# Kernel optimization log

Measured on AMD Instinct MI355X. Metric: run time of the kernel, lower is better.

## Reference

```python
import jax, jax.numpy as jnp
import numpy as np

B, M, N_CTR, K = 16, 2048, 512, 32
DIM, DEPTH, HEADS = 384, 6, 6
EMB = 48  # fourier embedding dim (48//6 = 8 freqs per axis, basis [3,24])


def make_basis():
    e = (2.0 ** np.arange(EMB // 6)).astype(np.float32) * np.pi  # [8]
    z = np.zeros(EMB // 6, np.float32)
    basis = np.stack([np.concatenate([e, z, z]),
                      np.concatenate([z, e, z]),
                      np.concatenate([z, z, e])])  # [3, 24]
    return jnp.asarray(basis)


def fourier_embed(x, basis):
    # x [..., 3] -> [..., 48]  (sin/cos of 24 frequency projections)
    p = jnp.einsum('...d,de->...e', x, basis)
    return jnp.concatenate([jnp.sin(p), jnp.cos(p)], axis=-1)


def fps_idx(pos, n):
    # farthest point sampling, deterministic start at index 0. pos [M,3] -> [n]
    d0 = jnp.sum((pos - pos[0]) ** 2, -1)
    def step(d, _):
        i = jnp.argmax(d)
        d = jnp.minimum(d, jnp.sum((pos - pos[i]) ** 2, -1))
        return d, i
    _, idxs = jax.lax.scan(step, d0, None, length=n - 1)
    return jnp.concatenate([jnp.zeros(1, jnp.int32), idxs.astype(jnp.int32)])


def layernorm(x, g, b, eps=1e-6):
    m = jnp.mean(x, -1, keepdims=True)
    v = jnp.var(x, -1, keepdims=True)
    return (x - m) * jax.lax.rsqrt(v + eps) * g + b


def _lin(key, fi, fo):
    kw, kb = jax.random.split(key)
    w = jax.random.normal(kw, (fi, fo), jnp.float32) / np.sqrt(fi)
    b = jax.random.normal(kb, (fo,), jnp.float32) * 0.01
    return w, b


def setup_inputs() -> dict:
    key = jax.random.key(0)
    ks = jax.random.split(key, 16)
    pc = jax.random.uniform(ks[0], (B, M, 3), jnp.float32)
    embed_w, embed_b = _lin(ks[1], 3 + EMB, DIM)
    lw1, lb1 = _lin(ks[2], 3 + EMB, 256)
    lw2, lb2 = _lin(ks[3], 256, 256)
    gw1, gb1 = _lin(ks[4], 256, 256)
    gw2, gb2 = _lin(ks[5], 256, DIM)
    def stack_lin(k, fi, fo):
        kk = jax.random.split(k, DEPTH)
        ws, bs = zip(*[_lin(kk[i], fi, fo) for i in range(DEPTH)])
        return jnp.stack(ws), jnp.stack(bs)
    qkv_w, qkv_b = stack_lin(ks[6], DIM, 3 * DIM)
    proj_w, proj_b = stack_lin(ks[7], DIM, DIM)
    fc1_w, fc1_b = stack_lin(ks[8], DIM, 4 * DIM)
    fc2_w, fc2_b = stack_lin(ks[9], 4 * DIM, DIM)
    return dict(
        pc=pc, embed_w=embed_w, embed_b=embed_b,
        lw1=lw1, lb1=lb1, lw2=lw2, lb2=lb2,
        gw1=gw1, gb1=gb1, gw2=gw2, gb2=gb2,
        ln1_g=jnp.ones((DEPTH, DIM)), ln1_b=jnp.zeros((DEPTH, DIM)),
        qkv_w=qkv_w, qkv_b=qkv_b, proj_w=proj_w, proj_b=proj_b,
        gamma1=jax.random.normal(ks[10], (DEPTH, DIM)) * 0.1,
        ln2_g=jnp.ones((DEPTH, DIM)), ln2_b=jnp.zeros((DEPTH, DIM)),
        fc1_w=fc1_w, fc1_b=fc1_b, fc2_w=fc2_w, fc2_b=fc2_b,
        gamma2=jax.random.normal(ks[11], (DEPTH, DIM)) * 0.1,
        lnf_g=jnp.ones((DIM,)), lnf_b=jnp.zeros((DIM,)),
    )


def reference(pc, embed_w, embed_b, lw1, lb1, lw2, lb2, gw1, gb1, gw2, gb2,
              ln1_g, ln1_b, qkv_w, qkv_b, proj_w, proj_b, gamma1,
              ln2_g, ln2_b, fc1_w, fc1_b, fc2_w, fc2_b, gamma2, lnf_g, lnf_b):
    basis = make_basis()
    # --- FPS centers (per batch) ---
    idx = jax.vmap(lambda p: fps_idx(p, N_CTR))(pc)                 # [B,N]
    centers = jnp.take_along_axis(pc, idx[:, :, None], axis=1)      # [B,N,3]
    # --- KNN graph: for each center, K nearest of the M points ---
    d2 = jnp.sum((centers[:, :, None, :] - pc[:, None, :, :]) ** 2, -1)  # [B,N,M]
    _, nn_idx = jax.lax.top_k(-d2, K)                               # [B,N,K]
    # --- PointConv: gather -> local MLP -> max-scatter -> global MLP ---
    src = jax.vmap(lambda p, i: p[i])(pc, nn_idx)                   # [B,N,K,3]
    rel = src - centers[:, :, None, :]
    feat = jnp.concatenate([rel, fourier_embed(rel, basis)], -1)    # [B,N,K,51]
    h = jax.nn.relu(feat @ lw1 + lb1) @ lw2 + lb2                   # [B,N,K,256]
    h = jnp.max(h, axis=2)  # scatter_max over edges == max over K neighbors
    x = jax.nn.relu(h @ gw1 + gb1) @ gw2 + gb2                      # [B,N,DIM]
    # --- positional embedding tokens ---
    pe = jnp.concatenate([centers, fourier_embed(centers, basis)], -1) @ embed_w + embed_b
    x = x + pe
    # --- ViT blocks (pre-LN, LayerScale, eval mode: no dropout/droppath) ---
    hd = DIM // HEADS
    scale = hd ** -0.5
    for l in range(DEPTH):
        xn = layernorm(x, ln1_g[l], ln1_b[l])
        qkv = (xn @ qkv_w[l] + qkv_b[l]).reshape(B, N_CTR, 3, HEADS, hd)
        q, k, v = jnp.moveaxis(qkv, 2, 0)                           # [B,N,H,hd]
        att = jax.nn.softmax(jnp.einsum('bqhd,bkhd->bhqk', q, k) * scale, axis=-1)
        o = jnp.einsum('bhqk,bkhd->bqhd', att, v).reshape(B, N_CTR, DIM)
        x = x + gamma1[l] * (o @ proj_w[l] + proj_b[l])
        xn = layernorm(x, ln2_g[l], ln2_b[l])
        mlp = jax.nn.gelu(xn @ fc1_w[l] + fc1_b[l], approximate=False) @ fc2_w[l] + fc2_b[l]
        x = x + gamma2[l] * mlp
    out = layernorm(x, lnf_g, lnf_b)
    return out, centers
```

## Files before the change

### kernel.cpp

```cpp
#include <hip/hip_runtime.h>
#include <math.h>

#define NB 16
#define NM 2048
#define NCTR 512
#define NK 32
#define NDIM 384

typedef unsigned long long ull;
typedef unsigned int uint;
typedef unsigned short ushort;
typedef __attribute__((ext_vector_type(8))) short bf16x8;
typedef __attribute__((ext_vector_type(4))) float f32x4;

__device__ __forceinline__ float dist2_exact(float ax, float ay, float az,
                                             float bx, float by, float bz) {
  float dx = __fsub_rn(ax, bx);
  float dy = __fsub_rn(ay, by);
  float dz = __fsub_rn(az, bz);
  return __fadd_rn(__fadd_rn(__fmul_rn(dx, dx), __fmul_rn(dy, dy)),
                   __fmul_rn(dz, dz));
}

__device__ __forceinline__ float gelu_f(float x) {
  return 0.5f * x * (1.0f + erff(x * 0.70710678118654752f));
}

__device__ __forceinline__ ushort f2bf(float f) {
  uint u = __float_as_uint(f);
  return (ushort)((u + 0x7FFFu + ((u >> 16) & 1u)) >> 16);
}
__device__ __forceinline__ float bf2f(ushort h) {
  return __uint_as_float(((uint)h) << 16);
}

__device__ __forceinline__ void cvt8(float4 p, float4 q, uint4& hi, uint4& lo) {
  float v0 = p.x, v1 = p.y, v2 = p.z, v3 = p.w;
  float v4 = q.x, v5 = q.y, v6 = q.z, v7 = q.w;
  ushort h0 = f2bf(v0), h1 = f2bf(v1), h2 = f2bf(v2), h3 = f2bf(v3);
  ushort h4 = f2bf(v4), h5 = f2bf(v5), h6 = f2bf(v6), h7 = f2bf(v7);
  ushort l0 = f2bf(v0 - bf2f(h0)), l1 = f2bf(v1 - bf2f(h1));
  ushort l2 = f2bf(v2 - bf2f(h2)), l3 = f2bf(v3 - bf2f(h3));
  ushort l4 = f2bf(v4 - bf2f(h4)), l5 = f2bf(v5 - bf2f(h5));
  ushort l6 = f2bf(v6 - bf2f(h6)), l7 = f2bf(v7 - bf2f(h7));
  hi.x = (uint)h0 | ((uint)h1 << 16); hi.y = (uint)h2 | ((uint)h3 << 16);
  hi.z = (uint)h4 | ((uint)h5 << 16); hi.w = (uint)h6 | ((uint)h7 << 16);
  lo.x = (uint)l0 | ((uint)l1 << 16); lo.y = (uint)l2 | ((uint)l3 << 16);
  lo.z = (uint)l4 | ((uint)l5 << 16); lo.w = (uint)l6 | ((uint)l7 << 16);
}

__device__ __forceinline__ void split_store(float v, ushort* H, ushort* L,
                                            size_t off) {
  ushort hi = f2bf(v);
  H[off] = hi;
  L[off] = f2bf(v - bf2f(hi));
}

struct WAll {
  const float* src[8];
  ushort* dst[8];
  int K8[8];
  int N[8];
  int Ksrc[8];
  int blk0[9];
};

__global__ __launch_bounds__(256)
void fps_wconv(const float* __restrict__ pc, float* __restrict__ centers,
               WAll a) {
  __shared__ float4 pos4[NM];
  __shared__ ull red[2][4];
  if (blockIdx.x >= 16) {
    int bid = blockIdx.x - 16;
    int f = 0;
#pragma unroll
    for (int i = 1; i < 8; ++i) f += (bid >= a.blk0[i]);
    int K8 = a.K8[f], N = a.N[f], Ksrc = a.Ksrc[f];
    int c = (bid - a.blk0[f]) * 256 + threadIdx.x;
    if (c >= K8 * N) return;
    const float* W = a.src[f];
    ushort* out = a.dst[f];
    int kb = c / N, n = c - kb * N;
    float v[8];
#pragma unroll
    for (int i = 0; i < 8; ++i) {
      int row = kb * 8 + i;
      v[i] = (row < Ksrc) ? W[(size_t)row * N + n] : 0.f;
    }
    float4 p, q;
    p.x = v[0]; p.y = v[1]; p.z = v[2]; p.w = v[3];
    q.x = v[4]; q.y = v[5]; q.z = v[6]; q.w = v[7];
    uint4 hi, lo;
    cvt8(p, q, hi, lo);
    *(uint4*)(out + (size_t)c * 8) = hi;
    *(uint4*)(out + (size_t)(K8 * N + c) * 8) = lo;
    return;
  }
  int b = blockIdx.x;
  const float* pb = pc + (size_t)b * (NM * 3);
  int tid = threadIdx.x, lane = tid & 63, wv = tid >> 6;
  float px[8], py[8], pz[8];
#pragma unroll
  for (int i = 0; i < 8; ++i) {
    int p = tid + 256 * i;
    float x = pb[3 * p], y = pb[3 * p + 1], z = pb[3 * p + 2];
    px[i] = x; py[i] = y; pz[i] = z;
    pos4[p] = make_float4(x, y, z, 0.f);
  }
  __syncthreads();
  float* cb = centers + (size_t)b * (NCTR * 3);
  float4 s0 = pos4[0];
  float sx = s0.x, sy = s0.y, sz = s0.z;
  if (tid == 0) { cb[0] = sx; cb[1] = sy; cb[2] = sz; }
  float d[8];
  for (int n = 1; n < NCTR; ++n) {
    ull best = 0;
#pragma unroll
    for (int i = 0; i < 8; ++i) {
      int p = tid + 256 * i;
      float nd = dist2_exact(px[i], py[i], pz[i], sx, sy, sz);
      d[i] = (n == 1) ? nd : fminf(d[i], nd);
      ull key = ((ull)__float_as_uint(d[i]) << 32) | (unsigned)(0x7FFFFFFF - p);
      best = best > key ? best : key;
    }
    float dl = __uint_as_float((uint)(best >> 32));
    float wm = dl;
#pragma unroll
    for (int off = 32; off; off >>= 1) wm = fmaxf(wm, __shfl_xor(wm, off));
    ull mask = __ballot(dl == wm);
    ull wkey;
    if (mask & (mask - 1)) {
      wkey = best;
#pragma unroll
      for (int off = 32; off; off >>= 1) {
        ull o = __shfl_xor(wkey, off);
        wkey = wkey > o ? wkey : o;
      }
    } else {
      int src = __ffsll((long long)mask) - 1;
      wkey = __shfl(best, src);
    }
    if (lane == 0) red[n & 1][wv] = wkey;
    __syncthreads();
    ull g0 = red[n & 1][0], g1 = red[n & 1][1];
    ull g2 = red[n & 1][2], g3 = red[n & 1][3];
    ull ga = g0 > g1 ? g0 : g1;
    ull gc2 = g2 > g3 ? g2 : g3;
    ull gb = ga > gc2 ? ga : gc2;
    int j = 0x7FFFFFFF - (int)(unsigned)(gb & 0xFFFFFFFFull);
    float4 np = pos4[j];
    sx = np.x; sy = np.y; sz = np.z;
    if (tid == 0) { cb[n * 3] = sx; cb[n * 3 + 1] = sy; cb[n * 3 + 2] = sz; }
  }
}

__global__ __launch_bounds__(256, 2)
void knn_kernel(const float* __restrict__ pc, const float* __restrict__ centers,
                int* __restrict__ nn) {
  __shared__ float pos[NM * 3];
  int b = blockIdx.x >> 7;
  int n0 = (blockIdx.x & 127) << 2;
  const float* pb = pc + (size_t)b * (NM * 3);
  for (int i = threadIdx.x; i < NM * 3; i += 256) pos[i] = pb[i];
  __syncthreads();
  int wv = threadIdx.x >> 6, lane = threadIdx.x & 63;
  int gc = b * NCTR + n0 + wv;
  float cx = centers[gc * 3], cy = centers[gc * 3 + 1], cz = centers[gc * 3 + 2];
  ull key[32];
  ull gmin[4];
#pragma unroll
  for (int g = 0; g < 4; ++g) {
    gmin[g] = ~0ull;
#pragma unroll
    for (int i = 0; i < 8; ++i) {
      int r = g * 8 + i;
      int p = lane + (r << 6);
      float nd = dist2_exact(pos[3 * p], pos[3 * p + 1], pos[3 * p + 2], cx, cy, cz);
      key[r] = ((ull)__float_as_uint(nd) << 11) | (unsigned)p;
      gmin[g] = gmin[g] < key[r] ? gmin[g] : key[r];
    }
  }
  ull a01 = gmin[0] < gmin[1] ? gmin[0] : gmin[1];
  ull a23 = gmin[2] < gmin[3] ? gmin[2] : gmin[3];
  ull lmin = a01 < a23 ? a01 : a23;
  int* nnc = nn + (size_t)gc * NK;
  for (int round = 0; round < NK; ++round) {
    ull w = lmin;
#pragma unroll
    for (int off = 32; off; off >>= 1) {
      ull o = __shfl_xor(w, off);
      w = w < o ? w : o;
    }
    if (lmin == w) {
      nnc[round] = (int)(w & 2047ull);
#pragma unroll
      for (int g = 0; g < 4; ++g) {
        if (gmin[g] == w) {
          gmin[g] = ~0ull;
#pragma unroll
          for (int i = 0; i < 8; ++i) {
            int r = g * 8 + i;
            key[r] = (key[r] == w) ? ~0ull : key[r];
            gmin[g] = gmin[g] < key[r] ? gmin[g] : key[r];
          }
        }
      }
      ull b01 = gmin[0] < gmin[1] ? gmin[0] : gmin[1];
      ull b23 = gmin[2] < gmin[3] ? gmin[2] : gmin[3];
      lmin = b01 < b23 ? b01 : b23;
    }
  }
}

__global__ __launch_bounds__(256, 2)
void edge_mfma(const float* __restrict__ pc, const float* __restrict__ centers,
               const int* __restrict__ nn, const ushort* __restrict__ lw1s,
               const float* __restrict__ lb1, const ushort* __restrict__ lw2s,
               const float* __restrict__ lb2, ushort* __restrict__ hH,
               ushort* __restrict__ hL) {
  __shared__ __align__(16) ushort featH[4096], featL[4096];
  __shared__ __align__(16) ushort t1H[16384], t1L[16384];
  int tid = threadIdx.x;
  int w = tid >> 6, lane = tid & 63;
  int l15 = lane & 15, l4 = lane >> 4;
  int wbase = w << 6;
  {
    int e = tid >> 2, s = tid & 3;
    int ge = blockIdx.x * 64 + e;
    int c = ge >> 5;
    int b = c >> 9;
    int j = nn[ge];
    const float* sp = pc + ((size_t)b * NM + j) * 3;
    float rx = sp[0] - centers[c * 3];
    float ry = sp[1] - centers[c * 3 + 1];
    float rz = sp[2] - centers[c * 3 + 2];
    auto putk = [&](int k, float v) {
      ushort hi = f2bf(v);
      ushort lo = f2bf(v - bf2f(hi));
      int idx = ((k >> 3) * 64 + e) * 8 + (k & 7);
      featH[idx] = hi;
      featL[idx] = lo;
    };
    if (s < 3) {
      float r = (s == 0) ? rx : (s == 1) ? ry : rz;
#pragma unroll
      for (int f = 0; f < 8; ++f) {
        float ef = (float)(M_PI * (double)(1 << f));
        float p = r * ef;
        putk(3 + 8 * s + f, sinf(p));
        putk(27 + 8 * s + f, cosf(p));
      }
    } else {
      putk(0, rx);
      putk(1, ry);
      putk(2, rz);
#pragma unroll
      for (int k = 51; k < 64; ++k) putk(k, 0.f);
    }
  }
  __syncthreads();
  const ushort* lw1H = lw1s;
  const ushort* lw1L = lw1s + 8 * 256 * 8;
  f32x4 acc1[4][4];
#pragma unroll
  for (int i = 0; i < 4; ++i)
#pragma unroll
    for (int j = 0; j < 4; ++j) acc1[i][j] = (f32x4){0.f, 0.f, 0.f, 0.f};
#pragma unroll
  for (int ks = 0; ks < 2; ++ks) {
    bf16x8 ah[4], al[4];
#pragma unroll
    for (int fm = 0; fm < 4; ++fm) {
      int idx = ((ks * 4 + l4) * 64 + fm * 16 + l15) * 8;
      ah[fm] = *(const bf16x8*)&featH[idx];
      al[fm] = *(const bf16x8*)&featL[idx];
    }
#pragma unroll
    for (int fn = 0; fn < 4; ++fn) {
      int col = wbase + fn * 16 + l15;
      size_t boff = ((size_t)(ks * 4 + l4) * 256 + col) * 8;
      bf16x8 bh = *(const bf16x8*)(lw1H + boff);
      bf16x8 bl = *(const bf16x8*)(lw1L + boff);
#pragma unroll
      for (int fm = 0; fm < 4; ++fm) {
        acc1[fm][fn] = __builtin_amdgcn_mfma_f32_16x16x32_bf16(al[fm], bh, acc1[fm][fn], 0, 0, 0);
        acc1[fm][fn] = __builtin_amdgcn_mfma_f32_16x16x32_bf16(ah[fm], bl, acc1[fm][fn], 0, 0, 0);
        acc1[fm][fn] = __builtin_amdgcn_mfma_f32_16x16x32_bf16(ah[fm], bh, acc1[fm][fn], 0, 0, 0);
      }
    }
  }
#pragma unroll
  for (int fn = 0; fn < 4; ++fn) {
    int chan = wbase + fn * 16 + l15;
    float bias = lb1[chan];
    int kb = chan >> 3, k7 = chan & 7;
#pragma unroll
    for (int fm = 0; fm < 4; ++fm) {
#pragma unroll
      for (int r = 0; r < 4; ++r) {
        int edge = fm * 16 + l4 * 4 + r;
        float v = fmaxf(acc1[fm][fn][r] + bias, 0.f);
        ushort hi = f2bf(v);
        ushort lo = f2bf(v - bf2f(hi));
        int idx = (kb * 64 + edge) * 8 + k7;
        t1H[idx] = hi;
        t1L[idx] = lo;
      }
    }
  }
  __syncthreads();
  const ushort* lw2H = lw2s;
  const ushort* lw2L = lw2s + 32 * 256 * 8;
  f32x4 acc2[4][4];
#pragma unroll
  for (int i = 0; i < 4; ++i)
#pragma unroll
    for (int j = 0; j < 4; ++j) acc2[i][j] = (f32x4){0.f, 0.f, 0.f, 0.f};
#pragma unroll
  for (int ks = 0; ks < 8; ++ks) {
    bf16x8 ah[4], al[4];
#pragma unroll
    for (int fm = 0; fm < 4; ++fm) {
      int idx = ((ks * 4 + l4) * 64 + fm * 16 + l15) * 8;
      ah[fm] = *(const bf16x8*)&t1H[idx];
      al[fm] = *(const bf16x8*)&t1L[idx];
    }
#pragma unroll
    for (int fn = 0; fn < 4; ++fn) {
      int col = wbase + fn * 16 + l15;
      size_t boff = ((size_t)(ks * 4 + l4) * 256 + col) * 8;
      bf16x8 bh = *(const bf16x8*)(lw2H + boff);
      bf16x8 bl = *(const bf16x8*)(lw2L + boff);
#pragma unroll
      for (int fm = 0; fm < 4; ++fm) {
        acc2[fm][fn] = __builtin_amdgcn_mfma_f32_16x16x32_bf16(al[fm], bh, acc2[fm][fn], 0, 0, 0);
        acc2[fm][fn] = __builtin_amdgcn_mfma_f32_16x16x32_bf16(ah[fm], bl, acc2[fm][fn], 0, 0, 0);
        acc2[fm][fn] = __builtin_amdgcn_mfma_f32_16x16x32_bf16(ah[fm], bh, acc2[fm][fn], 0, 0, 0);
      }
    }
  }
#pragma unroll
  for (int fn = 0; fn < 4; ++fn) {
    int col = wbase + fn * 16 + l15;
    float m0 = -INFINITY, m1 = -INFINITY;
#pragma unroll
    for (int r = 0; r < 4; ++r) {
      m0 = fmaxf(m0, fmaxf(acc2[0][fn][r], acc2[1][fn][r]));
      m1 = fmaxf(m1, fmaxf(acc2[2][fn][r], acc2[3][fn][r]));
    }
    m0 = fmaxf(m0, __shfl_xor(m0, 16));
    m0 = fmaxf(m0, __shfl_xor(m0, 32));
    m1 = fmaxf(m1, __shfl_xor(m1, 16));
    m1 = fmaxf(m1, __shfl_xor(m1, 32));
    if (l4 == 0) {
      float bias = lb2[col];
      int c0 = blockIdx.x * 2;
      split_store(m0 + bias, hH, hL, (size_t)c0 * 256 + col);
      split_store(m1 + bias, hH, hL, (size_t)(c0 + 1) * 256 + col);
    }
  }
}

template <int EPI, int OUTS, int BM>
__global__ __launch_bounds__(256, 2)
void gemm_s(const ushort* __restrict__ AH, const ushort* __restrict__ AL,
            const ushort* __restrict__ Wh, const ushort* __restrict__ Wl,
            const float* __restrict__ bias, const float* __restrict__ gamma,
            const float* __restrict__ resid, float* __restrict__ C,
            ushort* __restrict__ CH, ushort* __restrict__ CL,
            int M, int N, int K) {
  constexpr int FN = (BM == 128) ? 4 : 2;
  __shared__ __align__(16) ushort Ah[BM * 32], Al[BM * 32];
  __shared__ __align__(16) ushort Bh[4096], Bl[4096];
  int tid = threadIdx.x;
  int bn = blockIdx.x << 7, bm = blockIdx.y * BM;
  int wid = tid >> 6, lane = tid & 63;
  int wr = (BM == 128) ? (wid >> 1) : 0;
  int wc = (BM == 128) ? (wid & 1) : wid;
  int l15 = lane & 15, l4 = lane >> 4;

  int arow = (BM == 128) ? (tid >> 1) : (tid & 63);
  int akb0 = (BM == 128) ? ((tid & 1) << 1) : (tid >> 6);
  const ushort* ApH = AH + (size_t)(bm + arow) * K + akb0 * 8;
  const ushort* ApL = AL + (size_t)(bm + arow) * K + akb0 * 8;
  int wkb = tid >> 7, wn = tid & 127;

  f32x4 acc[4][FN];
#pragma unroll
  for (int i = 0; i < 4; ++i)
#pragma unroll
    for (int j = 0; j < FN; ++j) acc[i][j] = (f32x4){0.f, 0.f, 0.f, 0.f};

  uint4 aH0 = *(const uint4*)(ApH);
  uint4 aL0 = *(const uint4*)(ApL);
  uint4 aH1, aL1;
  if (BM == 128) {
    aH1 = *(const uint4*)(ApH + 8);
    aL1 = *(const uint4*)(ApL + 8);
  }
  size_t wo1 = ((size_t)wkb * N + bn + wn) * 8;
  size_t wo2 = ((size_t)(wkb + 2) * N + bn + wn) * 8;
  uint4 w0 = *(const uint4*)(Wh + wo1);
  uint4 w1 = *(const uint4*)(Wh + wo2);
  uint4 w2 = *(const uint4*)(Wl + wo1);
  uint4 w3 = *(const uint4*)(Wl + wo2);

  int nkt = K >> 5;
  for (int kt = 0; kt < nkt; ++kt) {
    if (BM == 128) {
      *(uint4*)&Ah[(akb0 * 128 + arow) * 8] = aH0;
      *(uint4*)&Ah[((akb0 + 1) * 128 + arow) * 8] = aH1;
      *(uint4*)&Al[(akb0 * 128 + arow) * 8] = aL0;
      *(uint4*)&Al[((akb0 + 1) * 128 + arow) * 8] = aL1;
    } else {
      *(uint4*)&Ah[(akb0 * 64 + arow) * 8] = aH0;
      *(uint4*)&Al[(akb0 * 64 + arow) * 8] = aL0;
    }
    *(uint4*)&Bh[tid * 8] = w0;
    *(uint4*)&Bh[(tid + 256) * 8] = w1;
    *(uint4*)&Bl[tid * 8] = w2;
    *(uint4*)&Bl[(tid + 256) * 8] = w3;
    __syncthreads();
    if (kt + 1 < nkt) {
      aH0 = *(const uint4*)(ApH + (kt + 1) * 32);
      aL0 = *(const uint4*)(ApL + (kt + 1) * 32);
      if (BM == 128) {
        aH1 = *(const uint4*)(ApH + (kt + 1) * 32 + 8);
        aL1 = *(const uint4*)(ApL + (kt + 1) * 32 + 8);
      }
      size_t b1 = ((size_t)((kt + 1) * 4 + wkb) * N + bn + wn) * 8;
      size_t b2 = ((size_t)((kt + 1) * 4 + wkb + 2) * N + bn + wn) * 8;
      w0 = *(const uint4*)(Wh + b1);
      w1 = *(const uint4*)(Wh + b2);
      w2 = *(const uint4*)(Wl + b1);
      w3 = *(const uint4*)(Wl + b2);
    }
    bf16x8 ahf[4], alf[4];
#pragma unroll
    for (int fm = 0; fm < 4; ++fm) {
      int ci = l4 * BM + wr * 64 + fm * 16 + l15;
      ahf[fm] = *(bf16x8*)&Ah[ci * 8];
      alf[fm] = *(bf16x8*)&Al[ci * 8];
    }
#pragma unroll
    for (int fn = 0; fn < FN; ++fn) {
      int ci = l4 * 128 + wc * (FN * 16) + fn * 16 + l15;
      bf16x8 bh = *(bf16x8*)&Bh[ci * 8];
      bf16x8 bl = *(bf16x8*)&Bl[ci * 8];
#pragma unroll
      for (int fm = 0; fm < 4; ++fm) {
        acc[fm][fn] = __builtin_amdgcn_mfma_f32_16x16x32_bf16(alf[fm], bh, acc[fm][fn], 0, 0, 0);
        acc[fm][fn] = __builtin_amdgcn_mfma_f32_16x16x32_bf16(ahf[fm], bl, acc[fm][fn], 0, 0, 0);
        acc[fm][fn] = __builtin_amdgcn_mfma_f32_16x16x32_bf16(ahf[fm], bh, acc[fm][fn], 0, 0, 0);
      }
    }
    __syncthreads();
  }

#pragma unroll
  for (int fn = 0; fn < FN; ++fn) {
    int col = bn + wc * (FN * 16) + fn * 16 + l15;
    float bv = bias[col];
    float gv = (EPI == 3) ? gamma[col] : 0.f;
#pragma unroll
    for (int fm = 0; fm < 4; ++fm) {
      int row0 = bm + wr * 64 + fm * 16 + l4 * 4;
#pragma unroll
      for (int r = 0; r < 4; ++r) {
        float v = acc[fm][fn][r] + bv;
        if (EPI == 1) v = fmaxf(v, 0.f);
        else if (EPI == 2) v = gelu_f(v);
        else if (EPI == 3) v = resid[(size_t)(row0 + r) * N + col] + gv * v;
        size_t off = (size_t)(row0 + r) * N + col;
        if (OUTS == 0) C[off] = v;
        else split_store(v, CH, CL, off);
      }
    }
  }
}

__global__ __launch_bounds__(256)
void pe_add(const float* __restrict__ centers, const float* __restrict__ ew,
            const float* __restrict__ eb, float* x) {
  __shared__ float fc[51];
  int c = blockIdx.x, tid = threadIdx.x;
  if (tid < 24) {
    int a = tid >> 3, f = tid & 7;
    float coord = centers[c * 3 + a];
    float p = coord * (float)(M_PI * (double)(1 << f));
    fc[3 + tid] = sinf(p);
    fc[27 + tid] = cosf(p);
  } else if (tid < 27) {
    fc[tid - 24] = centers[c * 3 + (tid - 24)];
  }
  __syncthreads();
  for (int j = tid; j < NDIM; j += 256) {
    float acc = eb[j];
#pragma unroll
    for (int d = 0; d < 51; ++d) acc = fmaf(fc[d], ew[d * NDIM + j], acc);
    x[(size_t)c * NDIM + j] += acc;
  }
}

__global__ __launch_bounds__(256)
void ln_f32(const float* __restrict__ x, const float* __restrict__ g,
            const float* __restrict__ b, float* __restrict__ y) {
  int row = (blockIdx.x << 2) + (threadIdx.x >> 6);
  int lane = threadIdx.x & 63;
  const float* xr = x + (size_t)row * NDIM;
  float v[6];
#pragma unroll
  for (int i = 0; i < 6; ++i) v[i] = xr[lane + (i << 6)];
  float s = 0.f;
#pragma unroll
  for (int i = 0; i < 6; ++i) s += v[i];
#pragma unroll
  for (int off = 32; off; off >>= 1) s += __shfl_xor(s, off);
  float m = s / 384.f;
  float var = 0.f;
#pragma unroll
  for (int i = 0; i < 6; ++i) { float dd = v[i] - m; var += dd * dd; }
#pragma unroll
  for (int off = 32; off; off >>= 1) var += __shfl_xor(var, off);
  var = var / 384.f;
  float rs = 1.f / sqrtf(var + 1e-6f);
#pragma unroll
  for (int i = 0; i < 6; ++i) {
    int cc = lane + (i << 6);
    y[(size_t)row * NDIM + cc] = (v[i] - m) * rs * g[cc] + b[cc];
  }
}

__global__ __launch_bounds__(256)
void ln_split(const float* __restrict__ x, const float* __restrict__ g,
              const float* __restrict__ b, ushort* __restrict__ yH,
              ushort* __restrict__ yL) {
  int row = (blockIdx.x << 2) + (threadIdx.x >> 6);
  int lane = threadIdx.x & 63;
  const float* xr = x + (size_t)row * NDIM;
  float v[6];
#pragma unroll
  for (int i = 0; i < 6; ++i) v[i] = xr[lane + (i << 6)];
  float s = 0.f;
#pragma unroll
  for (int i = 0; i < 6; ++i) s += v[i];
#pragma unroll
  for (int off = 32; off; off >>= 1) s += __shfl_xor(s, off);
  float m = s / 384.f;
  float var = 0.f;
#pragma unroll
  for (int i = 0; i < 6; ++i) { float dd = v[i] - m; var += dd * dd; }
#pragma unroll
  for (int off = 32; off; off >>= 1) var += __shfl_xor(var, off);
  var = var / 384.f;
  float rs = 1.f / sqrtf(var + 1e-6f);
#pragma unroll
  for (int i = 0; i < 6; ++i) {
    int cc = lane + (i << 6);
    float yv = (v[i] - m) * rs * g[cc] + b[cc];
    split_store(yv, yH, yL, (size_t)row * NDIM + cc);
  }
}

__global__ __launch_bounds__(256, 2)
void attn_mfma(const ushort* __restrict__ FH, const ushort* __restrict__ FL,
               ushort* __restrict__ oH, ushort* __restrict__ oL) {
  __shared__ __align__(16) ushort kTH[4096], kTL[4096];
  __shared__ __align__(16) ushort vSH[4096], vSL[4096];
  __shared__ __align__(16) ushort pSH[8192], pSL[8192];
  int bi = blockIdx.x;
  int qt = bi & 3;
  int hh = (bi >> 2) % 6;
  int b = bi / 24;
  int tid = threadIdx.x;
  int w = tid >> 6, lane = tid & 63;
  int l15 = lane & 15, l4 = lane >> 4;
  const ushort* baseH = FH + (size_t)(b * NCTR) * 1152;
  const ushort* baseL = FL + (size_t)(b * NCTR) * 1152;
  int qbase = qt * 128 + w * 32;

  bf16x8 qh[2][2], ql[2][2];
#pragma unroll
  for (int qr = 0; qr < 2; ++qr) {
#pragma unroll
    for (int ds = 0; ds < 2; ++ds) {
      size_t off = (size_t)(qbase + qr * 16 + l15) * 1152 + hh * 64 + ds * 32 + l4 * 8;
      qh[qr][ds] = *(const bf16x8*)(baseH + off);
      ql[qr][ds] = *(const bf16x8*)(baseL + off);
    }
  }

  f32x4 oacc[2][4];
#pragma unroll
  for (int i = 0; i < 2; ++i)
#pragma unroll
    for (int j = 0; j < 4; ++j) oacc[i][j] = (f32x4){0.f, 0.f, 0.f, 0.f};
  float m_[2][4], l_[2][4];
#pragma unroll
  for (int i = 0; i < 2; ++i)
#pragma unroll
    for (int r = 0; r < 4; ++r) { m_[i][r] = -INFINITY; l_[i][r] = 0.f; }

  ushort* pHw = pSH + w * 2048;
  ushort* pLw = pSL + w * 2048;

  for (int ch = 0; ch < 8; ++ch) {
    {
      int key = tid & 63, dgh = tid >> 6;
      size_t krow = (size_t)(ch * 64 + key) * 1152 + 384 + hh * 64;
#pragma unroll
      for (int i = 0; i < 2; ++i) {
        int dg = dgh * 2 + i;
        *(uint4*)&kTH[(dg * 64 + key) * 8] = *(const uint4*)(baseH + krow + dg * 8);
        *(uint4*)&kTL[(dg * 64 + key) * 8] = *(const uint4*)(baseL + krow + dg * 8);
      }
      int d = tid & 63, kb2 = tid >> 6;
#pragma unroll
      for (int i = 0; i < 2; ++i) {
        int kb = kb2 + i * 4;
        ushort hv[8], lv[8];
#pragma unroll
        for (int j = 0; j < 8; ++j) {
          size_t off = (size_t)(ch * 64 + kb * 8 + j) * 1152 + 768 + hh * 64 + d;
          hv[j] = baseH[off];
          lv[j] = baseL[off];
        }
        uint4 H, L;
        H.x = (uint)hv[0] | ((uint)hv[1] << 16); H.y = (uint)hv[2] | ((uint)hv[3] << 16);
        H.z = (uint)hv[4] | ((uint)hv[5] << 16); H.w = (uint)hv[6] | ((uint)hv[7] << 16);
        L.x = (uint)lv[0] | ((uint)lv[1] << 16); L.y = (uint)lv[2] | ((uint)lv[3] << 16);
        L.z = (uint)lv[4] | ((uint)lv[5] << 16); L.w = (uint)lv[6] | ((uint)lv[7] << 16);
        *(uint4*)&vSH[(kb * 64 + d) * 8] = H;
        *(uint4*)&vSL[(kb * 64 + d) * 8] = L;
      }
    }
    __syncthreads();

    f32x4 sacc[2][4];
#pragma unroll
    for (int i = 0; i < 2; ++i)
#pragma unroll
      for (int j = 0; j < 4; ++j) sacc[i][j] = (f32x4){0.f, 0.f, 0.f, 0.f};
#pragma unroll
    for (int ds = 0; ds < 2; ++ds) {
#pragma unroll
      for (int kc = 0; kc < 4; ++kc) {
        int idx = ((ds * 4 + l4) * 64 + kc * 16 + l15) * 8;
        bf16x8 bh = *(const bf16x8*)&kTH[idx];
        bf16x8 bl = *(const bf16x8*)&kTL[idx];
#pragma unroll
        for (int qr = 0; qr < 2; ++qr) {
          sacc[qr][kc] = __builtin_amdgcn_mfma_f32_16x16x32_bf16(ql[qr][ds], bh, sacc[qr][kc], 0, 0, 0);
          sacc[qr][kc] = __builtin_amdgcn_mfma_f32_16x16x32_bf16(qh[qr][ds], bl, sacc[qr][kc], 0, 0, 0);
          sacc[qr][kc] = __builtin_amdgcn_mfma_f32_16x16x32_bf16(qh[qr][ds], bh, sacc[qr][kc], 0, 0, 0);
        }
      }
    }

    float t[2][4];
#pragma unroll
    for (int qr = 0; qr < 2; ++qr)
#pragma unroll
      for (int r = 0; r < 4; ++r) {
        float a0 = sacc[qr][0][r] * 0.125f; sacc[qr][0][r] = a0;
        float a1 = sacc[qr][1][r] * 0.125f; sacc[qr][1][r] = a1;
        float a2 = sacc[qr][2][r] * 0.125f; sacc[qr][2][r] = a2;
        float a3 = sacc[qr][3][r] * 0.125f; sacc[qr][3][r] = a3;
        t[qr][r] = fmaxf(fmaxf(a0, a1), fmaxf(a2, a3));
      }
#pragma unroll
    for (int off = 1; off < 16; off <<= 1)
#pragma unroll
      for (int qr = 0; qr < 2; ++qr)
#pragma unroll
        for (int r = 0; r < 4; ++r)
          t[qr][r] = fmaxf(t[qr][r], __shfl_xor(t[qr][r], off));
    float f_[2][4];
#pragma unroll
    for (int qr = 0; qr < 2; ++qr)
#pragma unroll
      for (int r = 0; r < 4; ++r) {
        float mn = fmaxf(m_[qr][r], t[qr][r]);
        f_[qr][r] = expf(m_[qr][r] - mn);
        m_[qr][r] = mn;
      }
#pragma unroll
    for (int qr = 0; qr < 2; ++qr)
#pragma unroll
      for (int dc = 0; dc < 4; ++dc)
#pragma unroll
        for (int r = 0; r < 4; ++r) oacc[qr][dc][r] *= f_[qr][r];
    float sm[2][4];
#pragma unroll
    for (int qr = 0; qr < 2; ++qr)
#pragma unroll
      for (int r = 0; r < 4; ++r) {
        float p0 = expf(sacc[qr][0][r] - m_[qr][r]); sacc[qr][0][r] = p0;
        float p1 = expf(sacc[qr][1][r] - m_[qr][r]); sacc[qr][1][r] = p1;
        float p2 = expf(sacc[qr][2][r] - m_[qr][r]); sacc[qr][2][r] = p2;
        float p3 = expf(sacc[qr][3][r] - m_[qr][r]); sacc[qr][3][r] = p3;
        sm[qr][r] = ((p0 + p1) + (p2 + p3));
      }
#pragma unroll
    for (int off = 1; off < 16; off <<= 1)
#pragma unroll
      for (int qr = 0; qr < 2; ++qr)
#pragma unroll
        for (int r = 0; r < 4; ++r)
          sm[qr][r] += __shfl_xor(sm[qr][r], off);
#pragma unroll
    for (int qr = 0; qr < 2; ++qr)
#pragma unroll
      for (int r = 0; r < 4; ++r) l_[qr][r] = l_[qr][r] * f_[qr][r] + sm[qr][r];

#pragma unroll
    for (int qr = 0; qr < 2; ++qr)
#pragma unroll
      for (int kc = 0; kc < 4; ++kc)
#pragma unroll
        for (int r = 0; r < 4; ++r) {
          float pv = sacc[qr][kc][r];
          ushort hi = f2bf(pv);
          ushort lo = f2bf(pv - bf2f(hi));
          int k = kc * 16 + l15;
          int qrow = qr * 16 + l4 * 4 + r;
          int idx = ((k >> 3) * 32 + qrow) * 8 + (k & 7);
          pHw[idx] = hi;
          pLw[idx] = lo;
        }

#pragma unroll
    for (int ks = 0; ks < 2; ++ks) {
      bf16x8 pah[2], pal[2];
#pragma unroll
      for (int qr = 0; qr < 2; ++qr) {
        int idx = ((ks * 4 + l4) * 32 + qr * 16 + l15) * 8;
        pah[qr] = *(const bf16x8*)&pHw[idx];
        pal[qr] = *(const bf16x8*)&pLw[idx];
      }
#pragma unroll
      for (int dc = 0; dc < 4; ++dc) {
        int idx = ((ks * 4 + l4) * 64 + dc * 16 + l15) * 8;
        bf16x8 vh = *(const bf16x8*)&vSH[idx];
        bf16x8 vl = *(const bf16x8*)&vSL[idx];
#pragma unroll
        for (int qr = 0; qr < 2; ++qr) {
          oacc[qr][dc] = __builtin_amdgcn_mfma_f32_16x16x32_bf16(pal[qr], vh, oacc[qr][dc], 0, 0, 0);
          oacc[qr][dc] = __builtin_amdgcn_mfma_f32_16x16x32_bf16(pah[qr], vl, oacc[qr][dc], 0, 0, 0);
          oacc[qr][dc] = __builtin_amdgcn_mfma_f32_16x16x32_bf16(pah[qr], vh, oacc[qr][dc], 0, 0, 0);
        }
      }
    }
    __syncthreads();
  }

  float il[2][4];
#pragma unroll
  for (int qr = 0; qr < 2; ++qr)
#pragma unroll
    for (int r = 0; r < 4; ++r) il[qr][r] = 1.f / l_[qr][r];
#pragma unroll
  for (int qr = 0; qr < 2; ++qr)
#pragma unroll
    for (int dc = 0; dc < 4; ++dc)
#pragma unroll
      for (int r = 0; r < 4; ++r) {
        int row = b * NCTR + qbase + qr * 16 + l4 * 4 + r;
        int col = hh * 64 + dc * 16 + l15;
        split_store(oacc[qr][dc][r] * il[qr][r], oH, oL, (size_t)row * NDIM + col);
      }
}

extern "C" void kernel_launch(void* const* d_in, const int* in_sizes, int n_in,
                              void* d_out, int out_size, void* d_ws, size_t ws_size,
                              hipStream_t stream) {
  const float* pc      = (const float*)d_in[0];
  const float* embed_w = (const float*)d_in[1];
  const float* embed_b = (const float*)d_in[2];
  const float* lw1     = (const float*)d_in[3];
  const float* lb1     = (const float*)d_in[4];
  const float* lw2     = (const float*)d_in[5];
  const float* lb2     = (const float*)d_in[6];
  const float* gw1     = (const float*)d_in[7];
  const float* gb1     = (const float*)d_in[8];
  const float* gw2     = (const float*)d_in[9];
  const float* gb2     = (const float*)d_in[10];
  const float* ln1_g   = (const float*)d_in[11];
  const float* ln1_b   = (const float*)d_in[12];
  const float* qkv_w   = (const float*)d_in[13];
  const float* qkv_b   = (const float*)d_in[14];
  const float* proj_w  = (const float*)d_in[15];
  const float* proj_b  = (const float*)d_in[16];
  const float* gamma1  = (const float*)d_in[17];
  const float* ln2_g   = (const float*)d_in[18];
  const float* ln2_b   = (const float*)d_in[19];
  const float* fc1_w   = (const float*)d_in[20];
  const float* fc1_b   = (const float*)d_in[21];
  const float* fc2_w   = (const float*)d_in[22];
  const float* fc2_b   = (const float*)d_in[23];
  const float* gamma2  = (const float*)d_in[24];
  const float* lnf_g   = (const float*)d_in[25];
  const float* lnf_b   = (const float*)d_in[26];

  float* out = (float*)d_out;
  float* centers = out + (size_t)NB * NCTR * NDIM;

  char* ws = (char*)d_ws;
  int*    nn  = (int*)(ws + 0);
  float*  x   = (float*)(ws + 1048576);
  ushort* xnH = (ushort*)(ws + 13631488);
  ushort* xnL = (ushort*)(ws + 19922944);
  ushort* FH  = (ushort*)(ws + 26214400);
  ushort* FL  = (ushort*)(ws + 51380224);
  ushort* hH  = (ushort*)(ws + 76546048);
  ushort* hL  = (ushort*)(ws + 80740352);
  ushort* wsplit = (ushort*)(ws + 84934656);

  WAll wa;
  const float* srcs[8] = {qkv_w, proj_w, fc1_w, fc2_w, gw1, gw2, lw1, lw2};
  int kpads[8] = {2304, 2304, 2304, 9216, 256, 256, 64, 256};
  int ns[8]    = {1152, 384, 1536, 384, 256, 384, 256, 256};
  int ksrcs[8] = {2304, 2304, 2304, 9216, 256, 256, 51, 256};
  ushort* dsts[8];
  size_t wofs = 0;
  int cum = 0;
  for (int f = 0; f < 8; ++f) {
    dsts[f] = wsplit + wofs;
    wofs += (size_t)2 * kpads[f] * ns[f];
    wa.src[f] = srcs[f];
    wa.dst[f] = dsts[f];
    wa.K8[f] = kpads[f] >> 3;
    wa.N[f] = ns[f];
    wa.Ksrc[f] = ksrcs[f];
    wa.blk0[f] = cum;
    cum += ((kpads[f] >> 3) * ns[f] + 255) / 256;
  }
  wa.blk0[8] = cum;
  ushort* qkvS = dsts[0];
  ushort* projS = dsts[1];
  ushort* fc1S = dsts[2];
  ushort* fc2S = dsts[3];
  ushort* g1S = dsts[4];
  ushort* g2S = dsts[5];
  ushort* lw1s = dsts[6];
  ushort* lw2s = dsts[7];

  fps_wconv<<<16 + cum, 256, 0, stream>>>(pc, centers, wa);
  knn_kernel<<<2048, 256, 0, stream>>>(pc, centers, nn);
  edge_mfma<<<4096, 256, 0, stream>>>(pc, centers, nn, lw1s, lb1, lw2s, lb2, hH, hL);

  gemm_s<1, 1, 64><<<dim3(2, 128), 256, 0, stream>>>(
      hH, hL, g1S, g1S + 65536, gb1, nullptr, nullptr, nullptr, xnH, xnL,
      8192, 256, 256);
  gemm_s<0, 0, 64><<<dim3(3, 128), 256, 0, stream>>>(
      xnH, xnL, g2S, g2S + 98304, gb2, nullptr, nullptr, x, nullptr, nullptr,
      8192, 384, 256);
  pe_add<<<8192, 256, 0, stream>>>(centers, embed_w, embed_b, x);

  for (int l = 0; l < 6; ++l) {
    ln_split<<<2048, 256, 0, stream>>>(x, ln1_g + l * 384, ln1_b + l * 384, xnH, xnL);
    gemm_s<0, 1, 128><<<dim3(9, 64), 256, 0, stream>>>(
        xnH, xnL, qkvS + (size_t)l * 442368, qkvS + 2654208 + (size_t)l * 442368,
        qkv_b + l * 1152, nullptr, nullptr, nullptr, FH, FL, 8192, 1152, 384);
    attn_mfma<<<384, 256, 0, stream>>>(FH, FL, xnH, xnL);
    gemm_s<3, 0, 64><<<dim3(3, 128), 256, 0, stream>>>(
        xnH, xnL, projS + (size_t)l * 147456, projS + 884736 + (size_t)l * 147456,
        proj_b + l * 384, gamma1 + l * 384, x, x, nullptr, nullptr, 8192, 384, 384);
    ln_split<<<2048, 256, 0, stream>>>(x, ln2_g + l * 384, ln2_b + l * 384, xnH, xnL);
    gemm_s<2, 1, 128><<<dim3(12, 64), 256, 0, stream>>>(
        xnH, xnL, fc1S + (size_t)l * 589824, fc1S + 3538944 + (size_t)l * 589824,
        fc1_b + l * 1536, nullptr, nullptr, nullptr, FH, FL, 8192, 1536, 384);
    gemm_s<3, 0, 64><<<dim3(3, 128), 256, 0, stream>>>(
        FH, FL, fc2S + (size_t)l * 589824, fc2S + 3538944 + (size_t)l * 589824,
        fc2_b + l * 384, gamma2 + l * 384, x, x, nullptr, nullptr, 8192, 384, 1536);
  }
  ln_f32<<<2048, 256, 0, stream>>>(x, lnf_g, lnf_b, out);
}
```

Before: 1.985 ms.

## Fuse LayerNorm into QKV and FC1 GEMMs, reading fp32 activations directly

Removes the separate ln_split kernels and adds a gemm_ln kernel. Each block computes per-row mean and variance for its 128 rows, then normalizes and splits the fp32 input into hi/lo bf16 while staging the A tile in shared memory. This saves a kernel launch and the write and read of the bf16 normalized buffers twice per layer. In exchange every column block re-reads the fp32 rows and recomputes the statistics (9 or 12 times per row), variance now uses E[x^2]-m^2 which is less numerically robust, and the A load is fp32, so twice the bytes of bf16.

```diff
diff --git a/kernel.cpp b/kernel.cpp
--- a/kernel.cpp
+++ b/kernel.cpp
@@ -479,6 +479,157 @@
   }
 }
 
+template <int EPI>
+__global__ __launch_bounds__(256, 2)
+void gemm_ln(const float* __restrict__ X, const float* __restrict__ lng,
+             const float* __restrict__ lnb,
+             const ushort* __restrict__ Wh, const ushort* __restrict__ Wl,
+             const float* __restrict__ bias,
+             ushort* __restrict__ CH, ushort* __restrict__ CL, int N) {
+  constexpr int K = 384;
+  __shared__ __align__(16) ushort Ah[4096], Al[4096], Bh[4096], Bl[4096];
+  __shared__ __align__(16) float gS[384], bS[384];
+  __shared__ float mS[128], rS[128], redS[512];
+  int tid = threadIdx.x;
+  int bn = blockIdx.x << 7, bm = blockIdx.y << 7;
+  int wid = tid >> 6, lane = tid & 63;
+  int wr = wid >> 1, wc = wid & 1;
+  int l15 = lane & 15, l4 = lane >> 4;
+
+  {
+    const float* xr = X + (size_t)(bm + (tid >> 1)) * K + (tid & 1) * 192;
+    float s = 0.f, s2 = 0.f;
+#pragma unroll
+    for (int i = 0; i < 48; ++i) {
+      float4 v = *(const float4*)(xr + i * 4);
+      s += ((v.x + v.y) + (v.z + v.w));
+      s2 += ((v.x * v.x + v.y * v.y) + (v.z * v.z + v.w * v.w));
+    }
+    redS[tid] = s;
+    redS[256 + tid] = s2;
+    for (int i = tid; i < 384; i += 256) { gS[i] = lng[i]; bS[i] = lnb[i]; }
+    __syncthreads();
+    if (tid < 128) {
+      float st = redS[2 * tid] + redS[2 * tid + 1];
+      float q = redS[256 + 2 * tid] + redS[256 + 2 * tid + 1];
+      float m = st / 384.f;
+      float var = q / 384.f - m * m;
+      mS[tid] = m;
+      rS[tid] = 1.f / sqrtf(var + 1e-6f);
+    }
+    __syncthreads();
+  }
+
+  int arow = tid >> 1, akb0 = (tid & 1) << 1;
+  const float* Ap = X + (size_t)(bm + arow) * K + (akb0 << 3);
+  float rowm = mS[arow], rowr = rS[arow];
+  int wkb = tid >> 7, wn = tid & 127;
+
+  f32x4 acc[4][4];
+#pragma unroll
+  for (int i = 0; i < 4; ++i)
+#pragma unroll
+    for (int j = 0; j < 4; ++j) acc[i][j] = (f32x4){0.f, 0.f, 0.f, 0.f};
+
+  float4 a0 = *(const float4*)(Ap + 0);
+  float4 a1 = *(const float4*)(Ap + 4);
+  float4 a2 = *(const float4*)(Ap + 8);
+  float4 a3 = *(const float4*)(Ap + 12);
+  size_t wo1 = ((size_t)wkb * N + bn + wn) * 8;
+  size_t wo2 = ((size_t)(wkb + 2) * N + bn + wn) * 8;
+  uint4 w0 = *(const uint4*)(Wh + wo1);
+  uint4 w1 = *(const uint4*)(Wh + wo2);
+  uint4 w2 = *(const uint4*)(Wl + wo1);
+  uint4 w3 = *(const uint4*)(Wl + wo2);
+
+  constexpr int nkt = K >> 5;
+  for (int kt = 0; kt < nkt; ++kt) {
+    int kb = kt * 32 + (akb0 << 3);
+    float4 g0 = *(const float4*)&gS[kb],     g1v = *(const float4*)&gS[kb + 4];
+    float4 g2v = *(const float4*)&gS[kb + 8], g3v = *(const float4*)&gS[kb + 12];
+    float4 b0 = *(const float4*)&bS[kb],     b1v = *(const float4*)&bS[kb + 4];
+    float4 b2v = *(const float4*)&bS[kb + 8], b3v = *(const float4*)&bS[kb + 12];
+    float4 n0, n1, n2, n3;
+    n0.x = (a0.x - rowm) * rowr * g0.x + b0.x;
+    n0.y = (a0.y - rowm) * rowr * g0.y + b0.y;
+    n0.z = (a0.z - rowm) * rowr * g0.z + b0.z;
+    n0.w = (a0.w - rowm) * rowr * g0.w + b0.w;
+    n1.x = (a1.x - rowm) * rowr * g1v.x + b1v.x;
+    n1.y = (a1.y - rowm) * rowr * g1v.y + b1v.y;
+    n1.z = (a1.z - rowm) * rowr * g1v.z + b1v.z;
+    n1.w = (a1.w - rowm) * rowr * g1v.w + b1v.w;
+    n2.x = (a2.x - rowm) * rowr * g2v.x + b2v.x;
+    n2.y = (a2.y - rowm) * rowr * g2v.y + b2v.y;
+    n2.z = (a2.z - rowm) * rowr * g2v.z + b2v.z;
+    n2.w = (a2.w - rowm) * rowr * g2v.w + b2v.w;
+    n3.x = (a3.x - rowm) * rowr * g3v.x + b3v.x;
+    n3.y = (a3.y - rowm) * rowr * g3v.y + b3v.y;
+    n3.z = (a3.z - rowm) * rowr * g3v.z + b3v.z;
+    n3.w = (a3.w - rowm) * rowr * g3v.w + b3v.w;
+    uint4 h0, l0, h1, l1;
+    cvt8(n0, n1, h0, l0);
+    cvt8(n2, n3, h1, l1);
+    *(uint4*)&Ah[(akb0 * 128 + arow) * 8] = h0;
+    *(uint4*)&Ah[((akb0 + 1) * 128 + arow) * 8] = h1;
+    *(uint4*)&Al[(akb0 * 128 + arow) * 8] = l0;
+    *(uint4*)&Al[((akb0 + 1) * 128 + arow) * 8] = l1;
+    *(uint4*)&Bh[tid * 8] = w0;
+    *(uint4*)&Bh[(tid + 256) * 8] = w1;
+    *(uint4*)&Bl[tid * 8] = w2;
+    *(uint4*)&Bl[(tid + 256) * 8] = w3;
+    __syncthreads();
+    if (kt + 1 < nkt) {
+      const float* Apn = Ap + (kt + 1) * 32;
+      a0 = *(const float4*)(Apn + 0);
+      a1 = *(const float4*)(Apn + 4);
+      a2 = *(const float4*)(Apn + 8);
+      a3 = *(const float4*)(Apn + 12);
+      size_t c1 = ((size_t)((kt + 1) * 4 + wkb) * N + bn + wn) * 8;
+      size_t c2 = ((size_t)((kt + 1) * 4 + wkb + 2) * N + bn + wn) * 8;
+      w0 = *(const uint4*)(Wh + c1);
+      w1 = *(const uint4*)(Wh + c2);
+      w2 = *(const uint4*)(Wl + c1);
+      w3 = *(const uint4*)(Wl + c2);
+    }
+    bf16x8 ahf[4], alf[4];
+#pragma unroll
+    for (int fm = 0; fm < 4; ++fm) {
+      int ci = l4 * 128 + wr * 64 + fm * 16 + l15;
+      ahf[fm] = *(bf16x8*)&Ah[ci * 8];
+      alf[fm] = *(bf16x8*)&Al[ci * 8];
+    }
+#pragma unroll
+    for (int fn = 0; fn < 4; ++fn) {
+      int ci = l4 * 128 + wc * 64 + fn * 16 + l15;
+      bf16x8 bh = *(bf16x8*)&Bh[ci * 8];
+      bf16x8 bl = *(bf16x8*)&Bl[ci * 8];
+#pragma unroll
+      for (int fm = 0; fm < 4; ++fm) {
+        acc[fm][fn] = __builtin_amdgcn_mfma_f32_16x16x32_bf16(alf[fm], bh, acc[fm][fn], 0, 0, 0);
+        acc[fm][fn] = __builtin_amdgcn_mfma_f32_16x16x32_bf16(ahf[fm], bl, acc[fm][fn], 0, 0, 0);
+        acc[fm][fn] = __builtin_amdgcn_mfma_f32_16x16x32_bf16(ahf[fm], bh, acc[fm][fn], 0, 0, 0);
+      }
+    }
+    __syncthreads();
+  }
+
+#pragma unroll
+  for (int fn = 0; fn < 4; ++fn) {
+    int col = bn + wc * 64 + fn * 16 + l15;
+    float bv = bias[col];
+#pragma unroll
+    for (int fm = 0; fm < 4; ++fm) {
+      int row0 = bm + wr * 64 + fm * 16 + l4 * 4;
+#pragma unroll
+      for (int r = 0; r < 4; ++r) {
+        float v = acc[fm][fn][r] + bv;
+        if (EPI == 2) v = gelu_f(v);
+        split_store(v, CH, CL, (size_t)(row0 + r) * N + col);
+      }
+    }
+  }
+}
+
 __global__ __launch_bounds__(256)
 void pe_add(const float* __restrict__ centers, const float* __restrict__ ew,
             const float* __restrict__ eb, float* x) {
@@ -528,37 +679,6 @@
   for (int i = 0; i < 6; ++i) {
     int cc = lane + (i << 6);
     y[(size_t)row * NDIM + cc] = (v[i] - m) * rs * g[cc] + b[cc];
-  }
-}
-
-__global__ __launch_bounds__(256)
-void ln_split(const float* __restrict__ x, const float* __restrict__ g,
-              const float* __restrict__ b, ushort* __restrict__ yH,
-              ushort* __restrict__ yL) {
-  int row = (blockIdx.x << 2) + (threadIdx.x >> 6);
-  int lane = threadIdx.x & 63;
-  const float* xr = x + (size_t)row * NDIM;
-  float v[6];
-#pragma unroll
-  for (int i = 0; i < 6; ++i) v[i] = xr[lane + (i << 6)];
-  float s = 0.f;
-#pragma unroll
-  for (int i = 0; i < 6; ++i) s += v[i];
-#pragma unroll
-  for (int off = 32; off; off >>= 1) s += __shfl_xor(s, off);
-  float m = s / 384.f;
-  float var = 0.f;
-#pragma unroll
-  for (int i = 0; i < 6; ++i) { float dd = v[i] - m; var += dd * dd; }
-#pragma unroll
-  for (int off = 32; off; off >>= 1) var += __shfl_xor(var, off);
-  var = var / 384.f;
-  float rs = 1.f / sqrtf(var + 1e-6f);
-#pragma unroll
-  for (int i = 0; i < 6; ++i) {
-    int cc = lane + (i << 6);
-    float yv = (v[i] - m) * rs * g[cc] + b[cc];
-    split_store(yv, yH, yL, (size_t)row * NDIM + cc);
   }
 }
 
@@ -858,18 +978,18 @@
   pe_add<<<8192, 256, 0, stream>>>(centers, embed_w, embed_b, x);
 
   for (int l = 0; l < 6; ++l) {
-    ln_split<<<2048, 256, 0, stream>>>(x, ln1_g + l * 384, ln1_b + l * 384, xnH, xnL);
-    gemm_s<0, 1, 128><<<dim3(9, 64), 256, 0, stream>>>(
-        xnH, xnL, qkvS + (size_t)l * 442368, qkvS + 2654208 + (size_t)l * 442368,
-        qkv_b + l * 1152, nullptr, nullptr, nullptr, FH, FL, 8192, 1152, 384);
+    gemm_ln<0><<<dim3(9, 64), 256, 0, stream>>>(
+        x, ln1_g + l * 384, ln1_b + l * 384,
+        qkvS + (size_t)l * 442368, qkvS + 2654208 + (size_t)l * 442368,
+        qkv_b + l * 1152, FH, FL, 1152);
     attn_mfma<<<384, 256, 0, stream>>>(FH, FL, xnH, xnL);
     gemm_s<3, 0, 64><<<dim3(3, 128), 256, 0, stream>>>(
         xnH, xnL, projS + (size_t)l * 147456, projS + 884736 + (size_t)l * 147456,
         proj_b + l * 384, gamma1 + l * 384, x, x, nullptr, nullptr, 8192, 384, 384);
-    ln_split<<<2048, 256, 0, stream>>>(x, ln2_g + l * 384, ln2_b + l * 384, xnH, xnL);
-    gemm_s<2, 1, 128><<<dim3(12, 64), 256, 0, stream>>>(
-        xnH, xnL, fc1S + (size_t)l * 589824, fc1S + 3538944 + (size_t)l * 589824,
-        fc1_b + l * 1536, nullptr, nullptr, nullptr, FH, FL, 8192, 1536, 384);
+    gemm_ln<2><<<dim3(12, 64), 256, 0, stream>>>(
+        x, ln2_g + l * 384, ln2_b + l * 384,
+        fc1S + (size_t)l * 589824, fc1S + 3538944 + (size_t)l * 589824,
+        fc1_b + l * 1536, FH, FL, 1536);
     gemm_s<3, 0, 64><<<dim3(3, 128), 256, 0, stream>>>(
         FH, FL, fc2S + (size_t)l * 589824, fc2S + 3538944 + (size_t)l * 589824,
         fc2_b + l * 384, gamma2 + l * 384, x, x, nullptr, nullptr, 8192, 384, 1536);
```

New measurement: 2.206 ms. +11.1%, slower.

## Run farthest point sampling in a single wavefront per batch to drop block barriers

Applied to the files above, without the earlier changes.

Farthest point sampling now uses one 64-lane wavefront per batch, each lane holding 32 points in registers, so the per-iteration cross-wave shared-memory reduction and __syncthreads disappear. The argmax is tracked as a float plus index with lowest-index tie-breaking instead of packed 64-bit keys. The weight-conversion blocks sharing the launch are resized to 64 threads. The cost is four times more serial distance work per lane on the critical path and higher register pressure, with launch_bounds set to one block.

```diff
diff --git a/kernel.cpp b/kernel.cpp
--- a/kernel.cpp
+++ b/kernel.cpp
@@ -65,18 +65,17 @@
   int blk0[9];
 };
 
-__global__ __launch_bounds__(256)
+__global__ __launch_bounds__(64, 1)
 void fps_wconv(const float* __restrict__ pc, float* __restrict__ centers,
                WAll a) {
   __shared__ float4 pos4[NM];
-  __shared__ ull red[2][4];
   if (blockIdx.x >= 16) {
     int bid = blockIdx.x - 16;
     int f = 0;
 #pragma unroll
     for (int i = 1; i < 8; ++i) f += (bid >= a.blk0[i]);
     int K8 = a.K8[f], N = a.N[f], Ksrc = a.Ksrc[f];
-    int c = (bid - a.blk0[f]) * 256 + threadIdx.x;
+    int c = (bid - a.blk0[f]) * 64 + threadIdx.x;
     if (c >= K8 * N) return;
     const float* W = a.src[f];
     ushort* out = a.dst[f];
@@ -97,60 +96,51 @@
     return;
   }
   int b = blockIdx.x;
+  int lane = threadIdx.x;
   const float* pb = pc + (size_t)b * (NM * 3);
-  int tid = threadIdx.x, lane = tid & 63, wv = tid >> 6;
-  float px[8], py[8], pz[8];
-#pragma unroll
-  for (int i = 0; i < 8; ++i) {
-    int p = tid + 256 * i;
+  float px[32], py[32], pz[32], d[32];
+#pragma unroll
+  for (int i = 0; i < 32; ++i) {
+    int p = lane + (i << 6);
     float x = pb[3 * p], y = pb[3 * p + 1], z = pb[3 * p + 2];
     px[i] = x; py[i] = y; pz[i] = z;
     pos4[p] = make_float4(x, y, z, 0.f);
   }
-  __syncthreads();
   float* cb = centers + (size_t)b * (NCTR * 3);
   float4 s0 = pos4[0];
   float sx = s0.x, sy = s0.y, sz = s0.z;
-  if (tid == 0) { cb[0] = sx; cb[1] = sy; cb[2] = sz; }
-  float d[8];
+  if (lane == 0) { cb[0] = sx; cb[1] = sy; cb[2] = sz; }
   for (int n = 1; n < NCTR; ++n) {
-    ull best = 0;
-#pragma unroll
-    for (int i = 0; i < 8; ++i) {
-      int p = tid + 256 * i;
+    float dmax = -INFINITY;
+    int idx = 0;
+#pragma unroll
+    for (int i = 0; i < 32; ++i) {
+      int p = lane + (i << 6);
       float nd = dist2_exact(px[i], py[i], pz[i], sx, sy, sz);
       d[i] = (n == 1) ? nd : fminf(d[i], nd);
-      ull key = ((ull)__float_as_uint(d[i]) << 32) | (unsigned)(0x7FFFFFFF - p);
-      best = best > key ? best : key;
-    }
-    float dl = __uint_as_float((uint)(best >> 32));
-    float wm = dl;
+      bool gt = d[i] > dmax;
+      dmax = gt ? d[i] : dmax;
+      idx = gt ? p : idx;
+    }
+    float wm = dmax;
 #pragma unroll
     for (int off = 32; off; off >>= 1) wm = fmaxf(wm, __shfl_xor(wm, off));
-    ull mask = __ballot(dl == wm);
-    ull wkey;
+    ull mask = __ballot(dmax == wm);
+    int widx;
     if (mask & (mask - 1)) {
-      wkey = best;
+      int cand = (dmax == wm) ? idx : 0x7FFFFFFF;
 #pragma unroll
       for (int off = 32; off; off >>= 1) {
-        ull o = __shfl_xor(wkey, off);
-        wkey = wkey > o ? wkey : o;
-      }
+        int o = __shfl_xor(cand, off);
+        cand = o < cand ? o : cand;
+      }
+      widx = cand;
     } else {
-      int src = __ffsll((long long)mask) - 1;
-      wkey = __shfl(best, src);
-    }
-    if (lane == 0) red[n & 1][wv] = wkey;
-    __syncthreads();
-    ull g0 = red[n & 1][0], g1 = red[n & 1][1];
-    ull g2 = red[n & 1][2], g3 = red[n & 1][3];
-    ull ga = g0 > g1 ? g0 : g1;
-    ull gc2 = g2 > g3 ? g2 : g3;
-    ull gb = ga > gc2 ? ga : gc2;
-    int j = 0x7FFFFFFF - (int)(unsigned)(gb & 0xFFFFFFFFull);
-    float4 np = pos4[j];
+      widx = __shfl(idx, __ffsll((long long)mask) - 1);
+    }
+    float4 np = pos4[widx];
     sx = np.x; sy = np.y; sz = np.z;
-    if (tid == 0) { cb[n * 3] = sx; cb[n * 3 + 1] = sy; cb[n * 3 + 2] = sz; }
+    if (lane == 0) { cb[n * 3] = sx; cb[n * 3 + 1] = sy; cb[n * 3 + 2] = sz; }
   }
 }
 
@@ -833,7 +823,7 @@
     wa.N[f] = ns[f];
     wa.Ksrc[f] = ksrcs[f];
     wa.blk0[f] = cum;
-    cum += ((kpads[f] >> 3) * ns[f] + 255) / 256;
+    cum += ((kpads[f] >> 3) * ns[f] + 63) / 64;
   }
   wa.blk0[8] = cum;
   ushort* qkvS = dsts[0];
@@ -845,7 +835,7 @@
   ushort* lw1s = dsts[6];
   ushort* lw2s = dsts[7];
 
-  fps_wconv<<<16 + cum, 256, 0, stream>>>(pc, centers, wa);
+  fps_wconv<<<16 + cum, 64, 0, stream>>>(pc, centers, wa);
   knn_kernel<<<2048, 256, 0, stream>>>(pc, centers, nn);
   edge_mfma<<<4096, 256, 0, stream>>>(pc, centers, nn, lw1s, lb1, lw2s, lb2, hH, hL);
 
```

Result: slower. 2.172 ms (+9.4%).
